# Kernel optimization log

Measured on AMD Instinct MI355X. Metric: run time of the kernel, lower is better.

The kernel has to match this reference:

```python
import jax, jax.numpy as jnp
import numpy as np

B, S, V, H = 1, 2048, 1024, 16
D = V // H  # head_size = 64


def setup_inputs() -> dict:
    key = jax.random.key(0)
    ks = jax.random.split(key, 7)
    s = 1.0 / np.sqrt(V)  # keep logits in a sane range
    return {
        "x": jax.random.normal(ks[0], (B, S, V), jnp.float32),
        "W_qkv": (jax.random.normal(ks[1], (3 * V, V), jnp.float32) * s),
        "W_out": (jax.random.normal(ks[2], (V, V), jnp.float32) * s),
        "W_pos": (jax.random.normal(ks[3], (V, V), jnp.float32) * s),
        "u_vec": (jax.random.normal(ks[4], (1, H, 1, D), jnp.float32) * 0.02),
        "v_vec": (jax.random.normal(ks[5], (1, H, 1, D), jnp.float32) * 0.02),
        "rel_embed": jax.random.normal(ks[6], (S, V), jnp.float32),
    }


def reference(x, W_qkv, W_out, W_pos, u_vec, v_vec, rel_embed):
    b, s, _ = x.shape
    # qkv projection (nn.Linear, no bias): x @ W.T, then split into q,k,v
    qkv = x @ W_qkv.T
    q, k, v = jnp.split(qkv, 3, axis=-1)
    to_heads = lambda t: t.reshape(b, s, H, D).transpose(0, 2, 1, 3)  # [B,H,S,D]
    q, k, v = to_heads(q), to_heads(k), to_heads(v)

    # content term: (q + u) @ k^T  -> [B,H,S,S]
    attn_dots = jnp.einsum('bhid,bhjd->bhij', q + u_vec, k)

    # relative-position term: Linear(rel_embed).T viewed as [H, D, S]
    rel = (rel_embed @ W_pos.T).T.reshape(H, D, s)
    query_posn = jnp.einsum('bhid,hdj->bhij', q + v_vec, rel)  # [B,H,S,S]

    # Transformer-XL style shift-gather: out[i, j] = in[i, (j - i - 1) mod S]
    col_idx = ((-jnp.arange(s))[:, None] + jnp.arange(s)[None, :] - 1) % s
    shifted = jnp.take_along_axis(query_posn, col_idx[None, None, :, :], axis=-1)

    causal_mask = jnp.triu(jnp.ones((s, s), dtype=bool), k=1)  # True above diagonal
    dots = jnp.where(causal_mask, -jnp.inf, attn_dots + shifted) / np.sqrt(D)
    scores = jax.nn.softmax(dots, axis=-1)

    attn = jnp.einsum('bhij,bhjd->bhid', scores, v)
    out = attn.transpose(0, 2, 1, 3).reshape(b, s, V) @ W_out.T
    return out
```

## Files before the change

kernel.cpp:

```cpp
#include <hip/hip_runtime.h>
#include <math.h>

#define S 2048
#define H 16
#define D 64
#define V 1024

typedef float f32x4 __attribute__((ext_vector_type(4)));
typedef __bf16 bf16x8 __attribute__((ext_vector_type(8)));
typedef unsigned short u16;

#define GLOBAL_AS __attribute__((address_space(1)))
#define LDS_AS __attribute__((address_space(3)))

__device__ __forceinline__ u16 f2bf(float x) {
    unsigned u = __float_as_uint(x);
    u = u + 0x7FFFu + ((u >> 16) & 1u);
    return (u16)(u >> 16);
}
__device__ __forceinline__ float bf2f(u16 b) {
    return __uint_as_float(((unsigned)b) << 16);
}

#if __has_builtin(__builtin_amdgcn_global_load_lds)
#define HAS_ASYNC 1
#endif

__device__ __forceinline__ void async_ld16(const u16* g, u16* ldsu, int lane) {
#ifdef HAS_ASYNC
    auto gp = reinterpret_cast<GLOBAL_AS void*>(reinterpret_cast<uintptr_t>(g));
    auto lp = reinterpret_cast<LDS_AS void*>(reinterpret_cast<uintptr_t>(ldsu));
    __builtin_amdgcn_global_load_lds(gp, lp, 16, 0, 0);
#else
    *(uint4*)((char*)ldsu + lane * 16) = *(const uint4*)g;
#endif
}

__global__ __launch_bounds__(256) void prep5(
    const float* __restrict__ a0, u16* __restrict__ b0, int n0,
    const float* __restrict__ a1, u16* __restrict__ b1, int n1,
    const float* __restrict__ a2, u16* __restrict__ b2, int n2,
    const float* __restrict__ a3, u16* __restrict__ b3, int n3,
    const float* __restrict__ a4, u16* __restrict__ b4, int n4)
{
    const int tot = n0 + n1 + n2 + n3 + n4;
    for (int i = blockIdx.x * 256 + threadIdx.x; i < tot; i += gridDim.x * 256) {
        const float* s; u16* d; int j = i;
        if (j < n0) { s = a0; d = b0; }
        else if ((j -= n0) < n1) { s = a1; d = b1; }
        else if ((j -= n1) < n2) { s = a2; d = b2; }
        else if ((j -= n2) < n3) { s = a3; d = b3; }
        else { j -= n3; s = a4; d = b4; }
        float4 f = ((const float4*)s)[j];
        ((ushort4*)d)[j] = make_ushort4(f2bf(f.x), f2bf(f.y), f2bf(f.z), f2bf(f.w));
    }
}

__global__ __launch_bounds__(256) void gemm_proj(
    const u16* __restrict__ x_h, const u16* __restrict__ rel_h,
    const u16* __restrict__ Wq_h, const u16* __restrict__ Wpos_h,
    u16* __restrict__ qk_h, u16* __restrict__ Vt_g, u16* __restrict__ P_h)
{
    __shared__ u16 A_s[128 * 32];
    __shared__ u16 B_s[128 * 32];

    const int bid = blockIdx.x;
    const bool g1 = bid < 384;
    const int m0 = (g1 ? (bid / 24) : ((bid - 384) / 8)) * 128;
    const int n0 = (g1 ? (bid % 24) : ((bid - 384) % 8)) * 128;
    const u16* Ag = g1 ? x_h : rel_h;
    const u16* Bg = g1 ? Wq_h : Wpos_h;

    const int tid = threadIdx.x;
    const int lane = tid & 63;
    const int w = tid >> 6;
    const int wm = (w & 1) * 64, wn = (w >> 1) * 64;
    const int fr = lane & 15;
    const int fq = lane >> 4;
    const int lr = lane >> 2, lc = (lane & 3) * 8;

    f32x4 acc[4][4] = {};

    for (int k0 = 0; k0 < 1024; k0 += 32) {
        __syncthreads();
#pragma unroll
        for (int i = 0; i < 2; ++i) {
            const int r0 = w * 32 + i * 16;
            async_ld16(Ag + (size_t)(m0 + r0 + lr) * 1024 + k0 + lc, A_s + r0 * 32, lane);
            async_ld16(Bg + (size_t)(n0 + r0 + lr) * 1024 + k0 + lc, B_s + r0 * 32, lane);
        }
        __syncthreads();

        bf16x8 a[4], b[4];
#pragma unroll
        for (int t = 0; t < 4; ++t) {
            a[t] = *(const bf16x8*)&A_s[(wm + t * 16 + fr) * 32 + fq * 8];
            b[t] = *(const bf16x8*)&B_s[(wn + t * 16 + fr) * 32 + fq * 8];
        }
#pragma unroll
        for (int mi = 0; mi < 4; ++mi)
#pragma unroll
            for (int ni = 0; ni < 4; ++ni)
                acc[mi][ni] = __builtin_amdgcn_mfma_f32_16x16x32_bf16(
                    a[mi], b[ni], acc[mi][ni], 0, 0, 0);
    }

    const int er = fq * 4;
    if (g1 && n0 >= 2048) {
#pragma unroll
        for (int mi = 0; mi < 4; ++mi)
#pragma unroll
            for (int ni = 0; ni < 4; ++ni) {
                const int col = n0 - 2048 + wn + ni * 16 + fr;
                const int mrow = m0 + wm + mi * 16 + er;
                *(ushort4*)&Vt_g[(size_t)col * 2048 + mrow] = make_ushort4(
                    f2bf(acc[mi][ni][0]), f2bf(acc[mi][ni][1]),
                    f2bf(acc[mi][ni][2]), f2bf(acc[mi][ni][3]));
            }
    } else {
        u16* Cb = g1 ? qk_h : P_h;
        const int ldc = g1 ? 2048 : 1024;
#pragma unroll
        for (int mi = 0; mi < 4; ++mi)
#pragma unroll
            for (int ni = 0; ni < 4; ++ni)
#pragma unroll
                for (int g = 0; g < 4; ++g)
                    Cb[(size_t)(m0 + wm + mi * 16 + er + g) * ldc + n0 + wn + ni * 16 + fr] =
                        f2bf(acc[mi][ni][g]);
    }
}

__global__ __launch_bounds__(256, 3) void attn_mfma(
    const u16* __restrict__ qk_h, const u16* __restrict__ Vt_g,
    const u16* __restrict__ P_h,
    const float* __restrict__ u_vec, const float* __restrict__ v_vec,
    u16* __restrict__ O_h)
{
    const int h = blockIdx.y;
    const int tile = ((blockIdx.y >> 3) & 1) ? blockIdx.x : (gridDim.x - 1 - blockIdx.x);
    const int i0 = tile * 64;
    const int tid = threadIdx.x;
    const int lane = tid & 63;
    const int w = tid >> 6;
    const int fr = lane & 15;
    const int fq = lane >> 4;

    __shared__ u16 K_s[64 * 72];
    __shared__ u16 Vt_s[64 * 72];
    __shared__ u16 P_s[128 * 72];
    __shared__ u16 p_s[64 * 72];

    bf16x8 qu[2], qv[2];
    {
        const int row = i0 + w * 16 + fr;
        const int base = h * 64 + fq * 8;
#pragma unroll
        for (int c = 0; c < 2; ++c) {
            bf16x8 q8 = *(const bf16x8*)(qk_h + (size_t)row * 2048 + base + c * 32);
            float4 u0 = *(const float4*)(u_vec + base + c * 32);
            float4 u1 = *(const float4*)(u_vec + base + c * 32 + 4);
            float4 v0 = *(const float4*)(v_vec + base + c * 32);
            float4 v1 = *(const float4*)(v_vec + base + c * 32 + 4);
            const float uf[8] = {u0.x, u0.y, u0.z, u0.w, u1.x, u1.y, u1.z, u1.w};
            const float vf[8] = {v0.x, v0.y, v0.z, v0.w, v1.x, v1.y, v1.z, v1.w};
#pragma unroll
            for (int j = 0; j < 8; ++j) {
                const float qf = (float)q8[j];
                qu[c][j] = (__bf16)(qf + uf[j]);
                qv[c][j] = (__bf16)(qf + vf[j]);
            }
        }
    }

    const int rKV = tid >> 2;
    const int cKV = (tid & 3) * 16;
    const int rP = tid >> 1;
    const int cP = (tid & 1) * 32;

    uint4 pfK0, pfK1, pfV0, pfV1, pfP0, pfP1, pfP2, pfP3;
    auto load_pf = [&](int j0) {
        const u16* kg = qk_h + (size_t)(j0 + rKV) * 2048 + 1024 + h * 64 + cKV;
        pfK0 = *(const uint4*)kg;
        pfK1 = *(const uint4*)(kg + 8);
        const u16* vg = Vt_g + (size_t)(h * 64 + rKV) * 2048 + j0 + cKV;
        pfV0 = *(const uint4*)vg;
        pfV1 = *(const uint4*)(vg + 8);
        int prow = S + j0 - i0 - 64 + rP;
        if (prow > S - 1) prow = S - 1;
        const u16* pg = P_h + (size_t)prow * 1024 + h * 64 + cP;
        pfP0 = *(const uint4*)pg;
        pfP1 = *(const uint4*)(pg + 8);
        pfP2 = *(const uint4*)(pg + 16);
        pfP3 = *(const uint4*)(pg + 24);
    };

    f32x4 O[4] = {};
    float l[4] = {};

    const int tbase = 3 - w;
    const int bsh = 15 - fq * 4;

    load_pf(0);

    for (int j0 = 0; j0 <= i0; j0 += 64) {
        __syncthreads();
        *(uint4*)&K_s[rKV * 72 + cKV] = pfK0;
        *(uint4*)&K_s[rKV * 72 + cKV + 8] = pfK1;
        *(uint4*)&Vt_s[rKV * 72 + cKV] = pfV0;
        *(uint4*)&Vt_s[rKV * 72 + cKV + 8] = pfV1;
        *(uint4*)&P_s[rP * 72 + cP] = pfP0;
        *(uint4*)&P_s[rP * 72 + cP + 8] = pfP1;
        *(uint4*)&P_s[rP * 72 + cP + 16] = pfP2;
        *(uint4*)&P_s[rP * 72 + cP + 24] = pfP3;
        if (j0 + 64 <= i0) load_pf(j0 + 64);
        __syncthreads();

        f32x4 accQK[4] = {};
        f32x4 accQP[5] = {};
#pragma unroll
        for (int c = 0; c < 2; ++c) {
            const int kk = c * 32 + fq * 8;
#pragma unroll
            for (int nt = 0; nt < 4; ++nt) {
                bf16x8 b = *(const bf16x8*)&K_s[(nt * 16 + fr) * 72 + kk];
                accQK[nt] = __builtin_amdgcn_mfma_f32_16x16x32_bf16(qu[c], b, accQK[nt], 0, 0, 0);
            }
#pragma unroll
            for (int t = 0; t < 5; ++t) {
                bf16x8 b = *(const bf16x8*)&P_s[((tbase + t) * 16 + fr) * 72 + kk];
                accQP[t] = __builtin_amdgcn_mfma_f32_16x16x32_bf16(qv[c], b, accQP[t], 0, 0, 0);
            }
        }

        float p[4][4];
#pragma unroll
        for (int nt = 0; nt < 4; ++nt)
#pragma unroll
            for (int g = 0; g < 4; ++g) {
                const int b = bsh - g;
                const int srcfr = fr + b;
                const int srcLane = (fq << 4) | (srcfr & 15);
                const float lo = __shfl(accQP[nt][g], srcLane, 64);
                const float hi = __shfl(accQP[nt + 1][g], srcLane, 64);
                const float qp = (srcfr < 16) ? lo : hi;
                const int rr = w * 16 + fq * 4 + g;
                const int j = nt * 16 + fr;
                const float s = (accQK[nt][g] + qp) * 0.125f;
                const float e = ((j0 + j) <= (i0 + rr)) ? __expf(s) : 0.f;
                p[nt][g] = e;
                l[g] += e;
            }
#pragma unroll
        for (int nt = 0; nt < 4; ++nt)
#pragma unroll
            for (int g = 0; g < 4; ++g)
                p_s[(w * 16 + fq * 4 + g) * 72 + nt * 16 + fr] = f2bf(p[nt][g]);

#pragma unroll
        for (int c = 0; c < 2; ++c) {
            const int kk = c * 32 + fq * 8;
            bf16x8 a = *(const bf16x8*)&p_s[(w * 16 + fr) * 72 + kk];
#pragma unroll
            for (int nt = 0; nt < 4; ++nt) {
                bf16x8 b = *(const bf16x8*)&Vt_s[(nt * 16 + fr) * 72 + kk];
                O[nt] = __builtin_amdgcn_mfma_f32_16x16x32_bf16(a, b, O[nt], 0, 0, 0);
            }
        }
    }

#pragma unroll
    for (int g = 0; g < 4; ++g)
#pragma unroll
        for (int off = 1; off < 16; off <<= 1)
            l[g] += __shfl_xor(l[g], off, 64);

#pragma unroll
    for (int nt = 0; nt < 4; ++nt)
#pragma unroll
        for (int g = 0; g < 4; ++g) {
            const int rr = w * 16 + fq * 4 + g;
            O_h[(size_t)(i0 + rr) * 1024 + h * 64 + nt * 16 + fr] = f2bf(O[nt][g] / l[g]);
        }
}

__global__ __launch_bounds__(256) void gemm_out(
    const u16* __restrict__ O_g, const u16* __restrict__ Wout_h,
    float* __restrict__ C)
{
    __shared__ u16 A_s[128 * 32];
    __shared__ u16 B_s[64 * 32];

    const int tid = threadIdx.x;
    const int lane = tid & 63;
    const int w = tid >> 6;
    const int m0 = blockIdx.y * 128, n0 = blockIdx.x * 64;
    const int wm = (w & 1) * 64, wn = (w >> 1) * 32;
    const int fr = lane & 15;
    const int fq = lane >> 4;
    const int lr = lane >> 2, lc = (lane & 3) * 8;

    f32x4 acc[4][2] = {};

    for (int k0 = 0; k0 < 1024; k0 += 32) {
        __syncthreads();
#pragma unroll
        for (int i = 0; i < 2; ++i) {
            const int r0 = w * 32 + i * 16;
            async_ld16(O_g + (size_t)(m0 + r0 + lr) * 1024 + k0 + lc, A_s + r0 * 32, lane);
        }
        async_ld16(Wout_h + (size_t)(n0 + w * 16 + lr) * 1024 + k0 + lc,
                   B_s + w * 16 * 32, lane);
        __syncthreads();

        bf16x8 a[4], b[2];
#pragma unroll
        for (int t = 0; t < 4; ++t)
            a[t] = *(const bf16x8*)&A_s[(wm + t * 16 + fr) * 32 + fq * 8];
#pragma unroll
        for (int t = 0; t < 2; ++t)
            b[t] = *(const bf16x8*)&B_s[(wn + t * 16 + fr) * 32 + fq * 8];
#pragma unroll
        for (int mi = 0; mi < 4; ++mi)
#pragma unroll
            for (int ni = 0; ni < 2; ++ni)
                acc[mi][ni] = __builtin_amdgcn_mfma_f32_16x16x32_bf16(
                    a[mi], b[ni], acc[mi][ni], 0, 0, 0);
    }

    const int er = fq * 4;
#pragma unroll
    for (int mi = 0; mi < 4; ++mi)
#pragma unroll
        for (int ni = 0; ni < 2; ++ni)
#pragma unroll
            for (int g = 0; g < 4; ++g)
                C[(size_t)(m0 + wm + mi * 16 + er + g) * 1024 + n0 + wn + ni * 16 + fr] =
                    acc[mi][ni][g];
}

extern "C" void kernel_launch(void* const* d_in, const int* in_sizes, int n_in,
                              void* d_out, int out_size, void* d_ws, size_t ws_size,
                              hipStream_t stream) {
    const float* x     = (const float*)d_in[0];
    const float* W_qkv = (const float*)d_in[1];
    const float* W_out = (const float*)d_in[2];
    const float* W_pos = (const float*)d_in[3];
    const float* u_vec = (const float*)d_in[4];
    const float* v_vec = (const float*)d_in[5];
    const float* rel   = (const float*)d_in[6];
    float* out = (float*)d_out;

    char* ws = (char*)d_ws;
    u16* x_h    = (u16*)(ws);
    u16* rel_h  = (u16*)(ws + 4194304);
    u16* Wq_h   = (u16*)(ws + 8388608);
    u16* Wpos_h = (u16*)(ws + 14680064);
    u16* Wout_h = (u16*)(ws + 16777216);
    u16* qk_h   = (u16*)(ws + 18874368);
    u16* Vt_g   = (u16*)(ws + 27262976);
    u16* P_h    = (u16*)(ws + 31457280);
    u16* O_h    = (u16*)(ws + 35651584);

    prep5<<<dim3(2048), dim3(256), 0, stream>>>(
        x, x_h, 2048 * 1024 / 4,
        rel, rel_h, 2048 * 1024 / 4,
        W_qkv, Wq_h, 3072 * 1024 / 4,
        W_pos, Wpos_h, 1024 * 1024 / 4,
        W_out, Wout_h, 1024 * 1024 / 4);

    gemm_proj<<<dim3(512), dim3(256), 0, stream>>>(
        x_h, rel_h, Wq_h, Wpos_h, qk_h, Vt_g, P_h);

    attn_mfma<<<dim3(32, 16), dim3(256), 0, stream>>>(
        qk_h, Vt_g, P_h, u_vec, v_vec, O_h);

    gemm_out<<<dim3(16, 16), dim3(256), 0, stream>>>(O_h, Wout_h, out);
}
```

Baseline: 196.2 us.

## Split long causal query tiles across two blocks and merge partials in output GEMM

The attention grid grows so the 16 longest query tiles per head are each handled by two blocks that walk alternating 64-key chunks. Each writes an unnormalized partial output in bf16 plus its row sums into workspace reused from the dead x/rel buffers. The output GEMM adds the two partials and normalizes while loading its A tile, which fixes the causal load imbalance and shortens the critical path. The projection and output GEMMs also switch to smaller tiles so more blocks run. The cost is extra partial-output traffic, a non-async, conversion-heavy A load in gemm_out, and some bf16 rounding on unnormalized sums.

Result: no change. 196.6 us (+0.2%).

```diff
diff --git a/kernel.cpp b/kernel.cpp
--- a/kernel.cpp
+++ b/kernel.cpp
@@ -62,24 +62,24 @@
     u16* __restrict__ qk_h, u16* __restrict__ Vt_g, u16* __restrict__ P_h)
 {
     __shared__ u16 A_s[128 * 32];
-    __shared__ u16 B_s[128 * 32];
+    __shared__ u16 B_s[64 * 32];
 
     const int bid = blockIdx.x;
-    const bool g1 = bid < 384;
-    const int m0 = (g1 ? (bid / 24) : ((bid - 384) / 8)) * 128;
-    const int n0 = (g1 ? (bid % 24) : ((bid - 384) % 8)) * 128;
+    const bool g1 = bid < 768;
+    const int m0 = (g1 ? (bid / 48) : ((bid - 768) / 16)) * 128;
+    const int n0 = (g1 ? (bid % 48) : ((bid - 768) % 16)) * 64;
     const u16* Ag = g1 ? x_h : rel_h;
     const u16* Bg = g1 ? Wq_h : Wpos_h;
 
     const int tid = threadIdx.x;
     const int lane = tid & 63;
     const int w = tid >> 6;
-    const int wm = (w & 1) * 64, wn = (w >> 1) * 64;
+    const int wm = (w & 1) * 64, wn = (w >> 1) * 32;
     const int fr = lane & 15;
     const int fq = lane >> 4;
     const int lr = lane >> 2, lc = (lane & 3) * 8;
 
-    f32x4 acc[4][4] = {};
+    f32x4 acc[4][2] = {};
 
     for (int k0 = 0; k0 < 1024; k0 += 32) {
         __syncthreads();
@@ -87,20 +87,21 @@
         for (int i = 0; i < 2; ++i) {
             const int r0 = w * 32 + i * 16;
             async_ld16(Ag + (size_t)(m0 + r0 + lr) * 1024 + k0 + lc, A_s + r0 * 32, lane);
-            async_ld16(Bg + (size_t)(n0 + r0 + lr) * 1024 + k0 + lc, B_s + r0 * 32, lane);
-        }
-        __syncthreads();
-
-        bf16x8 a[4], b[4];
-#pragma unroll
-        for (int t = 0; t < 4; ++t) {
+        }
+        async_ld16(Bg + (size_t)(n0 + w * 16 + lr) * 1024 + k0 + lc, B_s + w * 16 * 32, lane);
+        __syncthreads();
+
+        bf16x8 a[4], b[2];
+#pragma unroll
+        for (int t = 0; t < 4; ++t)
             a[t] = *(const bf16x8*)&A_s[(wm + t * 16 + fr) * 32 + fq * 8];
+#pragma unroll
+        for (int t = 0; t < 2; ++t)
             b[t] = *(const bf16x8*)&B_s[(wn + t * 16 + fr) * 32 + fq * 8];
-        }
 #pragma unroll
         for (int mi = 0; mi < 4; ++mi)
 #pragma unroll
-            for (int ni = 0; ni < 4; ++ni)
+            for (int ni = 0; ni < 2; ++ni)
                 acc[mi][ni] = __builtin_amdgcn_mfma_f32_16x16x32_bf16(
                     a[mi], b[ni], acc[mi][ni], 0, 0, 0);
     }
@@ -110,7 +111,7 @@
 #pragma unroll
         for (int mi = 0; mi < 4; ++mi)
 #pragma unroll
-            for (int ni = 0; ni < 4; ++ni) {
+            for (int ni = 0; ni < 2; ++ni) {
                 const int col = n0 - 2048 + wn + ni * 16 + fr;
                 const int mrow = m0 + wm + mi * 16 + er;
                 *(ushort4*)&Vt_g[(size_t)col * 2048 + mrow] = make_ushort4(
@@ -123,7 +124,7 @@
 #pragma unroll
         for (int mi = 0; mi < 4; ++mi)
 #pragma unroll
-            for (int ni = 0; ni < 4; ++ni)
+            for (int ni = 0; ni < 2; ++ni)
 #pragma unroll
                 for (int g = 0; g < 4; ++g)
                     Cb[(size_t)(m0 + wm + mi * 16 + er + g) * ldc + n0 + wn + ni * 16 + fr] =
@@ -135,11 +136,16 @@
     const u16* __restrict__ qk_h, const u16* __restrict__ Vt_g,
     const u16* __restrict__ P_h,
     const float* __restrict__ u_vec, const float* __restrict__ v_vec,
-    u16* __restrict__ O_h)
+    u16* __restrict__ O_h, u16* __restrict__ Oh0, u16* __restrict__ Oh1,
+    float* __restrict__ L0, float* __restrict__ L1)
 {
     const int h = blockIdx.y;
-    const int tile = ((blockIdx.y >> 3) & 1) ? blockIdx.x : (gridDim.x - 1 - blockIdx.x);
-    const int i0 = tile * 64;
+    const int x = blockIdx.x;
+    const bool big = x < 32;
+    const int t = big ? 16 + (x >> 1) : 47 - x;
+    const int z = big ? (x & 1) : 0;
+    const int step = big ? 128 : 64;
+    const int i0 = t * 64;
     const int tid = threadIdx.x;
     const int lane = tid & 63;
     const int w = tid >> 6;
@@ -201,9 +207,9 @@
     const int tbase = 3 - w;
     const int bsh = 15 - fq * 4;
 
-    load_pf(0);
-
-    for (int j0 = 0; j0 <= i0; j0 += 64) {
+    load_pf(z * 64);
+
+    for (int j0 = z * 64; j0 <= i0; j0 += step) {
         __syncthreads();
         *(uint4*)&K_s[rKV * 72 + cKV] = pfK0;
         *(uint4*)&K_s[rKV * 72 + cKV + 8] = pfK1;
@@ -213,7 +219,7 @@
         *(uint4*)&P_s[rP * 72 + cP + 8] = pfP1;
         *(uint4*)&P_s[rP * 72 + cP + 16] = pfP2;
         *(uint4*)&P_s[rP * 72 + cP + 24] = pfP3;
-        if (j0 + 64 <= i0) load_pf(j0 + 64);
+        if (j0 + step <= i0) load_pf(j0 + step);
         __syncthreads();
 
         f32x4 accQK[4] = {};
@@ -227,9 +233,9 @@
                 accQK[nt] = __builtin_amdgcn_mfma_f32_16x16x32_bf16(qu[c], b, accQK[nt], 0, 0, 0);
             }
 #pragma unroll
-            for (int t = 0; t < 5; ++t) {
-                bf16x8 b = *(const bf16x8*)&P_s[((tbase + t) * 16 + fr) * 72 + kk];
-                accQP[t] = __builtin_amdgcn_mfma_f32_16x16x32_bf16(qv[c], b, accQP[t], 0, 0, 0);
+            for (int tt = 0; tt < 5; ++tt) {
+                bf16x8 b = *(const bf16x8*)&P_s[((tbase + tt) * 16 + fr) * 72 + kk];
+                accQP[tt] = __builtin_amdgcn_mfma_f32_16x16x32_bf16(qv[c], b, accQP[tt], 0, 0, 0);
             }
         }
 
@@ -275,53 +281,89 @@
         for (int off = 1; off < 16; off <<= 1)
             l[g] += __shfl_xor(l[g], off, 64);
 
-#pragma unroll
-    for (int nt = 0; nt < 4; ++nt)
-#pragma unroll
-        for (int g = 0; g < 4; ++g) {
-            const int rr = w * 16 + fq * 4 + g;
-            O_h[(size_t)(i0 + rr) * 1024 + h * 64 + nt * 16 + fr] = f2bf(O[nt][g] / l[g]);
-        }
+    if (big) {
+        u16* Op = z ? Oh1 : Oh0;
+        float* Lp = z ? L1 : L0;
+#pragma unroll
+        for (int nt = 0; nt < 4; ++nt)
+#pragma unroll
+            for (int g = 0; g < 4; ++g) {
+                const int rr = w * 16 + fq * 4 + g;
+                Op[(size_t)(i0 + rr - 1024) * 1024 + h * 64 + nt * 16 + fr] = f2bf(O[nt][g]);
+            }
+        if (fr == 0)
+#pragma unroll
+            for (int g = 0; g < 4; ++g)
+                Lp[h * 2048 + i0 + w * 16 + fq * 4 + g] = l[g];
+    } else {
+#pragma unroll
+        for (int nt = 0; nt < 4; ++nt)
+#pragma unroll
+            for (int g = 0; g < 4; ++g) {
+                const int rr = w * 16 + fq * 4 + g;
+                O_h[(size_t)(i0 + rr) * 1024 + h * 64 + nt * 16 + fr] = f2bf(O[nt][g] / l[g]);
+            }
+    }
 }
 
 __global__ __launch_bounds__(256) void gemm_out(
-    const u16* __restrict__ O_g, const u16* __restrict__ Wout_h,
-    float* __restrict__ C)
+    const u16* __restrict__ O_g,
+    const u16* __restrict__ Oh0, const u16* __restrict__ Oh1,
+    const float* __restrict__ L0, const float* __restrict__ L1,
+    const u16* __restrict__ Wout_h, float* __restrict__ C)
 {
-    __shared__ u16 A_s[128 * 32];
+    __shared__ u16 A_s[64 * 32];
     __shared__ u16 B_s[64 * 32];
 
     const int tid = threadIdx.x;
     const int lane = tid & 63;
     const int w = tid >> 6;
-    const int m0 = blockIdx.y * 128, n0 = blockIdx.x * 64;
-    const int wm = (w & 1) * 64, wn = (w >> 1) * 32;
+    const int m0 = blockIdx.y * 64, n0 = blockIdx.x * 64;
+    const bool big = m0 >= 1024;
+    const int wm = (w & 1) * 32, wn = (w >> 1) * 32;
     const int fr = lane & 15;
     const int fq = lane >> 4;
     const int lr = lane >> 2, lc = (lane & 3) * 8;
-
-    f32x4 acc[4][2] = {};
+    const int arow = tid >> 2;
+    const int akc = (tid & 3) * 8;
+
+    f32x4 acc[2][2] = {};
 
     for (int k0 = 0; k0 < 1024; k0 += 32) {
         __syncthreads();
-#pragma unroll
-        for (int i = 0; i < 2; ++i) {
-            const int r0 = w * 32 + i * 16;
-            async_ld16(O_g + (size_t)(m0 + r0 + lr) * 1024 + k0 + lc, A_s + r0 * 32, lane);
+        if (big) {
+            const int grow = m0 + arow;
+            const int hh = (k0 + akc) >> 6;
+            const float linv = 1.f / (L0[hh * 2048 + grow] + L1[hh * 2048 + grow]);
+            const u16* p0 = Oh0 + (size_t)(grow - 1024) * 1024 + k0 + akc;
+            const u16* p1 = Oh1 + (size_t)(grow - 1024) * 1024 + k0 + akc;
+            u16* dst = A_s + arow * 32 + akc;
+#pragma unroll
+            for (int j = 0; j < 8; j += 4) {
+                ushort4 a4 = *(const ushort4*)(p0 + j);
+                ushort4 b4 = *(const ushort4*)(p1 + j);
+                *(ushort4*)(dst + j) = make_ushort4(
+                    f2bf((bf2f(a4.x) + bf2f(b4.x)) * linv),
+                    f2bf((bf2f(a4.y) + bf2f(b4.y)) * linv),
+                    f2bf((bf2f(a4.z) + bf2f(b4.z)) * linv),
+                    f2bf((bf2f(a4.w) + bf2f(b4.w)) * linv));
+            }
+        } else {
+            *(uint4*)&A_s[arow * 32 + akc] =
+                *(const uint4*)(O_g + (size_t)(m0 + arow) * 1024 + k0 + akc);
         }
         async_ld16(Wout_h + (size_t)(n0 + w * 16 + lr) * 1024 + k0 + lc,
                    B_s + w * 16 * 32, lane);
         __syncthreads();
 
-        bf16x8 a[4], b[2];
-#pragma unroll
-        for (int t = 0; t < 4; ++t)
+        bf16x8 a[2], b[2];
+#pragma unroll
+        for (int t = 0; t < 2; ++t) {
             a[t] = *(const bf16x8*)&A_s[(wm + t * 16 + fr) * 32 + fq * 8];
-#pragma unroll
-        for (int t = 0; t < 2; ++t)
             b[t] = *(const bf16x8*)&B_s[(wn + t * 16 + fr) * 32 + fq * 8];
-#pragma unroll
-        for (int mi = 0; mi < 4; ++mi)
+        }
+#pragma unroll
+        for (int mi = 0; mi < 2; ++mi)
 #pragma unroll
             for (int ni = 0; ni < 2; ++ni)
                 acc[mi][ni] = __builtin_amdgcn_mfma_f32_16x16x32_bf16(
@@ -330,7 +372,7 @@
 
     const int er = fq * 4;
 #pragma unroll
-    for (int mi = 0; mi < 4; ++mi)
+    for (int mi = 0; mi < 2; ++mi)
 #pragma unroll
         for (int ni = 0; ni < 2; ++ni)
 #pragma unroll
@@ -354,6 +396,10 @@
     char* ws = (char*)d_ws;
     u16* x_h    = (u16*)(ws);
     u16* rel_h  = (u16*)(ws + 4194304);
+    u16* Oh0    = (u16*)(ws);
+    u16* Oh1    = (u16*)(ws + 2097152);
+    float* L0   = (float*)(ws + 4194304);
+    float* L1   = (float*)(ws + 4325376);
     u16* Wq_h   = (u16*)(ws + 8388608);
     u16* Wpos_h = (u16*)(ws + 14680064);
     u16* Wout_h = (u16*)(ws + 16777216);
@@ -369,11 +415,12 @@
         W_pos, Wpos_h, 1024 * 1024 / 4,
         W_out, Wout_h, 1024 * 1024 / 4);
 
-    gemm_proj<<<dim3(512), dim3(256), 0, stream>>>(
+    gemm_proj<<<dim3(1024), dim3(256), 0, stream>>>(
         x_h, rel_h, Wq_h, Wpos_h, qk_h, Vt_g, P_h);
 
-    attn_mfma<<<dim3(32, 16), dim3(256), 0, stream>>>(
-        qk_h, Vt_g, P_h, u_vec, v_vec, O_h);
-
-    gemm_out<<<dim3(16, 16), dim3(256), 0, stream>>>(O_h, Wout_h, out);
-}
+    attn_mfma<<<dim3(48, 16), dim3(256), 0, stream>>>(
+        qk_h, Vt_g, P_h, u_vec, v_vec, O_h, Oh0, Oh1, L0, L1);
+
+    gemm_out<<<dim3(16, 32), dim3(256), 0, stream>>>(
+        O_h, Oh0, Oh1, L0, L1, Wout_h, out);
+}
```
